# Performance work log

Hardware: AMD Instinct MI355X
Metric: run time of the kernel (lower is better)

The kernel has to match this reference:

```python
import jax, jax.numpy as jnp
import numpy as np

B, IDF, CDF, SIZE, H, L = 32, 64, 256, 32, 8, 256
SS = SIZE * SIZE  # size*size = 1024


def setup_inputs() -> dict:
    key = jax.random.key(0)
    k1, k2, k3 = jax.random.split(key, 3)
    return {
        "weightedContext": jax.random.normal(k1, (B, IDF, SS), dtype=jnp.float32),
        "context": jax.random.normal(k2, (B, CDF, L), dtype=jnp.float32),
        # per-head conv1x1 weights: [H, size*size, cdf]
        "W": jax.random.normal(k3, (H, SS, CDF), dtype=jnp.float32) * 0.02,
        "ih": SIZE,
        "iw": SIZE,
    }


def reference(weightedContext, context, W, ih, iw):
    batch, idf = weightedContext.shape[0], weightedContext.shape[1]
    # conv1x1 per head == per-head GEMM over channel dim: [B,H,SS,L]
    sourceC = jnp.einsum("hoc,bcl->bhol", W, context)
    # attention scores: [B,H,idf,L]
    attn = jnp.einsum("bio,bhol->bhil", weightedContext, sourceC)
    # softmax over sourceL (nn.Softmax() on 2D view -> dim=1 == L here)
    attn = jax.nn.softmax(attn, axis=-1)
    # weightedContext_T summed over heads: bmm(sourceC, attn^T) -> [B,idf,SS]
    ctx_out = jnp.einsum("bhol,bhil->bio", sourceC, attn)
    ctx_out = ctx_out.reshape(batch, idf, ih, iw)
    # attnOut: per-head attn transposed [B,L,idf], summed over heads
    attn_out = jnp.sum(attn, axis=1).transpose(0, 2, 1)
    return ctx_out, attn_out
```

## Files before the change

### kernel.cpp

```cpp
#include <hip/hip_runtime.h>
#include <hip/hip_bf16.h>

#define BB 32
#define IDF 64
#define CDF 256
#define SSZ 1024
#define NH 8
#define LL 256
#define KHC 2048

typedef __attribute__((ext_vector_type(8))) _Float16 half8v;
typedef __attribute__((ext_vector_type(4))) float f32x4;

#define GLDS16(g, l) __builtin_amdgcn_global_load_lds(                        \
    (const __attribute__((address_space(1))) void*)(g),                       \
    (__attribute__((address_space(3))) void*)(l), 16, 0, 0)

#define WAIT_ENTER3(NFULL, NHALF)                                             \
  { if (ks < NSTEP - 2)                                                       \
      asm volatile("s_waitcnt vmcnt(" #NFULL ")" ::: "memory");               \
    else if (ks == NSTEP - 2)                                                 \
      asm volatile("s_waitcnt vmcnt(" #NHALF ")" ::: "memory");               \
    else                                                                      \
      asm volatile("s_waitcnt vmcnt(0)" ::: "memory");                        \
    __builtin_amdgcn_s_barrier();                                             \
    __builtin_amdgcn_sched_barrier(0); }
#define BAR_EXIT()                                                            \
  { __builtin_amdgcn_sched_barrier(0);                                        \
    __builtin_amdgcn_s_barrier();                                             \
    __builtin_amdgcn_sched_barrier(0); }

__device__ inline unsigned short f2h(float x) {
  _Float16 h = (_Float16)x;
  return *reinterpret_cast<unsigned short*>(&h);
}
__device__ inline float h2f(unsigned short u) {
  _Float16 h = *reinterpret_cast<_Float16*>(&u);
  return (float)h;
}

__global__ __launch_bounds__(256) void k_split_all(const float* __restrict__ wc,
                                                   const float* __restrict__ W,
                                                   const float* __restrict__ ctx,
                                                   unsigned short* __restrict__ wc16,
                                                   unsigned short* __restrict__ W16,
                                                   unsigned short* __restrict__ ctx16) {
  int sel = blockIdx.x >> 11;
  int idx = ((blockIdx.x & 2047) * 256 + threadIdx.x) * 4;
  const float* src = (sel == 0) ? wc : (sel == 1) ? W : ctx;
  unsigned short* d = (sel == 0) ? wc16 : (sel == 1) ? W16 : ctx16;
  float4 v = *reinterpret_cast<const float4*>(&src[idx]);
  __align__(8) unsigned short h[4] = {f2h(v.x), f2h(v.y), f2h(v.z), f2h(v.w)};
  *reinterpret_cast<int2*>(&d[idx]) = *reinterpret_cast<int2*>(h);
}

__global__ __launch_bounds__(256) void k_split_T(const float* __restrict__ W,
                                                 const float* __restrict__ ctx,
                                                 unsigned short* __restrict__ wt,
                                                 unsigned short* __restrict__ ct) {
  __shared__ float Tt[64][65];
  int blk0 = blockIdx.x;
  int t = threadIdx.x;
  if (blk0 < 512) {
    int blk = blk0;
    int h = blk >> 6, ot = (blk >> 2) & 15, cq = blk & 3;
    int og = ot * 64, cg = cq * 64;
    int o_l = t >> 4, c4 = (t & 15) * 4;
#pragma unroll
    for (int p = 0; p < 4; ++p) {
      int o = o_l + 16 * p;
      float4 v = *reinterpret_cast<const float4*>(
          &W[((size_t)h * SSZ + og + o) * CDF + cg + c4]);
      Tt[c4 + 0][o] = v.x; Tt[c4 + 1][o] = v.y;
      Tt[c4 + 2][o] = v.z; Tt[c4 + 3][o] = v.w;
    }
    __syncthreads();
    int c_l = t >> 2;
#pragma unroll
    for (int p = 0; p < 4; ++p) {
      int o0 = ((t & 3) + 4 * p) * 4;
      __align__(8) unsigned short hv[4];
#pragma unroll
      for (int j = 0; j < 4; ++j) hv[j] = f2h(Tt[c_l][o0 + j]);
      size_t base = ((size_t)h * CDF + cg + c_l) * SSZ + og + o0;
      *reinterpret_cast<int2*>(&wt[base]) = *reinterpret_cast<int2*>(hv);
    }
  } else {
    int blk = blk0 - 512;
    int b = blk >> 4, cq = (blk >> 2) & 3, lt = blk & 3;
    int cg = cq * 64, lg = lt * 64;
    int c_l = t >> 4, l4 = (t & 15) * 4;
#pragma unroll
    for (int p = 0; p < 4; ++p) {
      int c = c_l + 16 * p;
      float4 v = *reinterpret_cast<const float4*>(
          &ctx[((size_t)b * CDF + cg + c) * LL + lg + l4]);
      Tt[l4 + 0][c] = v.x; Tt[l4 + 1][c] = v.y;
      Tt[l4 + 2][c] = v.z; Tt[l4 + 3][c] = v.w;
    }
    __syncthreads();
    int l_l = t >> 2;
#pragma unroll
    for (int p = 0; p < 4; ++p) {
      int c0 = ((t & 3) + 4 * p) * 4;
      __align__(8) unsigned short hv[4];
#pragma unroll
      for (int j = 0; j < 4; ++j) hv[j] = f2h(Tt[l_l][c0 + j]);
      size_t base = ((size_t)b * LL + lg + l_l) * CDF + cg + c0;
      *reinterpret_cast<int2*>(&ct[base]) = *reinterpret_cast<int2*>(hv);
    }
  }
}

__device__ __forceinline__ void k1_stage(short* dst,
                                         const short* gA, const short* gB,
                                         int wave, int lane, int k0) {
#pragma unroll
  for (int j = 0; j < 3; ++j) {
    int inst = wave * 3 + j;
    if (inst < 4) {
      int rb = inst * 16;
      int r  = rb + (lane >> 2);
      int gc = (lane & 3) ^ ((r >> 1) & 3);
      GLDS16(gA + (size_t)r * SSZ + k0 + gc * 8, dst + rb * 32);
    } else {
      int rb = (inst - 4) * 16;
      int r  = rb + (lane >> 2);
      int gc = (lane & 3) ^ ((r >> 1) & 3);
      GLDS16(gB + (size_t)r * SSZ + k0 + gc * 8, dst + 2048 + rb * 32);
    }
  }
}

__global__ __launch_bounds__(256) void k1_mfma(const unsigned short* __restrict__ wc16,
                                               const unsigned short* __restrict__ Wt16,
                                               unsigned short* __restrict__ M16) {
  __shared__ __align__(16) short S[3 * 6144];

  int blk = blockIdx.x;
  int bh = blk >> 1, nh = blk & 1;
  int b = bh >> 3, h = bh & 7;
  int t = threadIdx.x;
  int lane = t & 63, wave = t >> 6;
  int ln15 = lane & 15, kh = lane >> 4;

  const short* gA = (const short*)wc16 + (size_t)b * IDF * SSZ;
  const short* gB = (const short*)Wt16 + (size_t)(h * CDF + nh * 128) * SSZ;

  int offA[4], offB[2];
#pragma unroll
  for (int r = 0; r < 4; ++r) {
    int row = r * 16 + ln15;
    offA[r] = row * 32 + ((kh ^ ((row >> 1) & 3)) * 8);
  }
#pragma unroll
  for (int c = 0; c < 2; ++c) {
    int row = wave * 32 + c * 16 + ln15;
    offB[c] = 2048 + row * 32 + ((kh ^ ((row >> 1) & 3)) * 8);
  }

  f32x4 acc[4][2] = {};
  k1_stage(&S[0],        gA, gB, wave, lane, 0);
  k1_stage(&S[6144],     gA, gB, wave, lane, 32);
  k1_stage(&S[2 * 6144], gA, gB, wave, lane, 64);
  int cur = 0;

  const int NSTEP = 32;
#pragma unroll 1
  for (int ks = 0; ks < NSTEP; ++ks) {
    short* Sc = &S[cur * 6144];
    WAIT_ENTER3(6, 3)
    half8v fa[4], fb[2];
#pragma unroll
    for (int r = 0; r < 4; ++r)
      fa[r] = *reinterpret_cast<const half8v*>(&Sc[offA[r]]);
#pragma unroll
    for (int c = 0; c < 2; ++c)
      fb[c] = *reinterpret_cast<const half8v*>(&Sc[offB[c]]);
    __builtin_amdgcn_s_setprio(1);
#pragma unroll
    for (int r = 0; r < 4; ++r)
#pragma unroll
      for (int c = 0; c < 2; ++c)
        acc[r][c] = __builtin_amdgcn_mfma_f32_16x16x32_f16(fa[r], fb[c], acc[r][c], 0, 0, 0);
    __builtin_amdgcn_s_setprio(0);
    BAR_EXIT()
    if (ks + 3 < NSTEP)
      k1_stage(Sc, gA, gB, wave, lane, (ks + 3) * 32);
    cur = (cur == 2) ? 0 : cur + 1;
  }

  size_t obase = (size_t)bh * IDF * CDF + nh * 128;
  int rowq = (lane >> 4) * 4;
#pragma unroll
  for (int r = 0; r < 4; ++r)
#pragma unroll
    for (int c = 0; c < 2; ++c)
#pragma unroll
      for (int reg = 0; reg < 4; ++reg) {
        size_t idx = obase + (size_t)(r * 16 + rowq + reg) * CDF + wave * 32 + c * 16 + ln15;
        M16[idx] = f2h(acc[r][c][reg]);
      }
}

__device__ __forceinline__ void k2_stage(short* dst,
                                         const short* gM, const short* gT,
                                         int wave, int lane, int k0) {
#pragma unroll
  for (int j = 0; j < 3; ++j) {
    int inst = wave * 3 + j;
    const short* src; int tile_off, rb;
    if (inst < 4)       { src = gM; tile_off = 0;     rb = inst * 16; }
    else if (inst < 20) { src = gT; tile_off = 2048;  rb = (inst - 4) * 16; }
    else                { src = gM; tile_off = 10240; rb = (inst - 20) * 16; }
    int r  = rb + (lane >> 2);
    int gc = (lane & 3) ^ ((r >> 1) & 3);
    GLDS16(src + (size_t)r * CDF + k0 + gc * 8, dst + tile_off + rb * 32);
  }
}

__global__ __launch_bounds__(512) void k_attn(const unsigned short* __restrict__ M16,
                                              const unsigned short* __restrict__ cT16,
                                              unsigned short* __restrict__ P16) {
  __shared__ __align__(16) short S[3 * 12288];

  int bh = blockIdx.x;
  int b = bh >> 3;
  int t = threadIdx.x;
  int lane = t & 63, wave = t >> 6;
  int ln15 = lane & 15, kh = lane >> 4;

  const short* gM = (const short*)M16 + (size_t)bh * IDF * CDF;
  const short* gT = (const short*)cT16 + (size_t)b * LL * CDF;

  int offA[4], offB[2];
#pragma unroll
  for (int r = 0; r < 4; ++r) {
    int row = r * 16 + ln15;
    offA[r] = row * 32 + ((kh ^ ((row >> 1) & 3)) * 8);
  }
#pragma unroll
  for (int c = 0; c < 2; ++c) {
    int row = wave * 32 + c * 16 + ln15;
    offB[c] = 2048 + row * 32 + ((kh ^ ((row >> 1) & 3)) * 8);
  }

  f32x4 acc[4][2] = {};
  k2_stage(&S[0],         gM, gT, wave, lane, 0);
  k2_stage(&S[12288],     gM, gT, wave, lane, 32);
  k2_stage(&S[2 * 12288], gM, gT, wave, lane, 64);
  int cur = 0;

  const int NSTEP = 8;
#pragma unroll 1
  for (int ks = 0; ks < NSTEP; ++ks) {
    short* Sc = &S[cur * 12288];
    WAIT_ENTER3(6, 3)
    half8v fa[4], fb[2];
#pragma unroll
    for (int r = 0; r < 4; ++r)
      fa[r] = *reinterpret_cast<const half8v*>(&Sc[offA[r]]);
#pragma unroll
    for (int c = 0; c < 2; ++c)
      fb[c] = *reinterpret_cast<const half8v*>(&Sc[offB[c]]);
    __builtin_amdgcn_s_setprio(1);
#pragma unroll
    for (int r = 0; r < 4; ++r)
#pragma unroll
      for (int c = 0; c < 2; ++c)
        acc[r][c] = __builtin_amdgcn_mfma_f32_16x16x32_f16(fa[r], fb[c], acc[r][c], 0, 0, 0);
    __builtin_amdgcn_s_setprio(0);
    BAR_EXIT()
    if (ks + 3 < NSTEP)
      k2_stage(Sc, gM, gT, wave, lane, (ks + 3) * 32);
    cur = (cur == 2) ? 0 : cur + 1;
  }

  float* pm = reinterpret_cast<float*>(&S[0]);
  int rowq = (lane >> 4) * 4;
  float gmax[4][4], ginv[4][4];
#pragma unroll
  for (int r = 0; r < 4; ++r)
#pragma unroll
    for (int reg = 0; reg < 4; ++reg) {
      float m = fmaxf(acc[r][0][reg], acc[r][1][reg]);
#pragma unroll
      for (int msk = 8; msk >= 1; msk >>= 1) m = fmaxf(m, __shfl_xor(m, msk, 64));
      if (ln15 == 0) pm[(r * 16 + rowq + reg) * 8 + wave] = m;
    }
  __syncthreads();
#pragma unroll
  for (int r = 0; r < 4; ++r)
#pragma unroll
    for (int reg = 0; reg < 4; ++reg) {
      int row = r * 16 + rowq + reg;
      float4 p0 = *reinterpret_cast<const float4*>(&pm[row * 8]);
      float4 p1 = *reinterpret_cast<const float4*>(&pm[row * 8 + 4]);
      gmax[r][reg] = fmaxf(fmaxf(fmaxf(p0.x, p0.y), fmaxf(p0.z, p0.w)),
                           fmaxf(fmaxf(p1.x, p1.y), fmaxf(p1.z, p1.w)));
    }
  __syncthreads();
#pragma unroll
  for (int r = 0; r < 4; ++r)
#pragma unroll
    for (int reg = 0; reg < 4; ++reg) {
      acc[r][0][reg] = __expf(acc[r][0][reg] - gmax[r][reg]);
      acc[r][1][reg] = __expf(acc[r][1][reg] - gmax[r][reg]);
      float s = acc[r][0][reg] + acc[r][1][reg];
#pragma unroll
      for (int msk = 8; msk >= 1; msk >>= 1) s += __shfl_xor(s, msk, 64);
      if (ln15 == 0) pm[(r * 16 + rowq + reg) * 8 + wave] = s;
    }
  __syncthreads();
#pragma unroll
  for (int r = 0; r < 4; ++r)
#pragma unroll
    for (int reg = 0; reg < 4; ++reg) {
      int row = r * 16 + rowq + reg;
      float4 p0 = *reinterpret_cast<const float4*>(&pm[row * 8]);
      float4 p1 = *reinterpret_cast<const float4*>(&pm[row * 8 + 4]);
      ginv[r][reg] = 1.f / (p0.x + p0.y + p0.z + p0.w + p1.x + p1.y + p1.z + p1.w);
    }
  size_t obase = (size_t)bh * IDF * LL;
#pragma unroll
  for (int r = 0; r < 4; ++r)
#pragma unroll
    for (int c = 0; c < 2; ++c)
#pragma unroll
      for (int reg = 0; reg < 4; ++reg) {
        float p = acc[r][c][reg] * ginv[r][reg];
        size_t idx = obase + (size_t)(r * 16 + rowq + reg) * LL + wave * 32 + c * 16 + ln15;
        P16[idx] = f2h(p);
      }
}

__device__ __forceinline__ void k3_stage(short* dst,
                                         const short* gP, const short* gC,
                                         int wave, int lane, int k0) {
#pragma unroll
  for (int j = 0; j < 3; ++j) {
    int inst = wave * 3 + j;
    const short* src; int tile_off, rb;
    if (inst < 4) { src = gP; tile_off = 0;    rb = inst * 16; }
    else          { src = gC; tile_off = 2048; rb = (inst - 4) * 16; }
    int r  = rb + (lane >> 2);
    int gc = (lane & 3) ^ ((r >> 1) & 3);
    GLDS16(src + (size_t)r * LL + k0 + gc * 8, dst + tile_off + rb * 32);
  }
}

__global__ __launch_bounds__(256) void k_N2(const unsigned short* __restrict__ P16,
                                            const unsigned short* __restrict__ ctx16,
                                            unsigned short* __restrict__ N216) {
  __shared__ __align__(16) short S[3 * 6144];

  int blk = blockIdx.x;
  int bh = blk >> 1, ch = blk & 1;
  int b = bh >> 3, h = bh & 7;
  int cgbase = ch * 128;
  int t = threadIdx.x;
  int lane = t & 63, wave = t >> 6;
  int ln15 = lane & 15, kh = lane >> 4;

  const short* gP = (const short*)P16 + (size_t)bh * IDF * LL;
  const short* gC = (const short*)ctx16 + (size_t)(b * CDF + cgbase) * LL;

  int offA[4], offB[2];
#pragma unroll
  for (int r = 0; r < 4; ++r) {
    int row = r * 16 + ln15;
    offA[r] = row * 32 + ((kh ^ ((row >> 1) & 3)) * 8);
  }
#pragma unroll
  for (int c = 0; c < 2; ++c) {
    int row = wave * 32 + c * 16 + ln15;
    offB[c] = 2048 + row * 32 + ((kh ^ ((row >> 1) & 3)) * 8);
  }

  f32x4 acc[4][2] = {};
  k3_stage(&S[0],        gP, gC, wave, lane, 0);
  k3_stage(&S[6144],     gP, gC, wave, lane, 32);
  k3_stage(&S[2 * 6144], gP, gC, wave, lane, 64);
  int cur = 0;

  const int NSTEP = 8;
#pragma unroll 1
  for (int ks = 0; ks < NSTEP; ++ks) {
    short* Sc = &S[cur * 6144];
    WAIT_ENTER3(6, 3)
    half8v fa[4], fb[2];
#pragma unroll
    for (int r = 0; r < 4; ++r)
      fa[r] = *reinterpret_cast<const half8v*>(&Sc[offA[r]]);
#pragma unroll
    for (int c = 0; c < 2; ++c)
      fb[c] = *reinterpret_cast<const half8v*>(&Sc[offB[c]]);
    __builtin_amdgcn_s_setprio(1);
#pragma unroll
    for (int r = 0; r < 4; ++r)
#pragma unroll
      for (int c = 0; c < 2; ++c)
        acc[r][c] = __builtin_amdgcn_mfma_f32_16x16x32_f16(fa[r], fb[c], acc[r][c], 0, 0, 0);
    __builtin_amdgcn_s_setprio(0);
    BAR_EXIT()
    if (ks + 3 < NSTEP)
      k3_stage(Sc, gP, gC, wave, lane, (ks + 3) * 32);
    cur = (cur == 2) ? 0 : cur + 1;
  }

  size_t base = (size_t)b * IDF * KHC + h * CDF + cgbase;
  int rowq = (lane >> 4) * 4;
#pragma unroll
  for (int r = 0; r < 4; ++r)
#pragma unroll
    for (int c = 0; c < 2; ++c)
#pragma unroll
      for (int reg = 0; reg < 4; ++reg) {
        size_t idx = base + (size_t)(r * 16 + rowq + reg) * KHC + wave * 32 + c * 16 + ln15;
        N216[idx] = f2h(acc[r][c][reg]);
      }
}

__device__ __forceinline__ void k4_stage(short* dst,
                                         const short* gA, const short* gB,
                                         int wave, int lane, int kk0, int obase) {
  int h4 = kk0 >> 8, cb = kk0 & 255;
#pragma unroll
  for (int j = 0; j < 3; ++j) {
    int inst = wave * 3 + j;
    if (inst < 4) {
      int rb = inst * 16;
      int r  = rb + (lane >> 2);
      int gc = (lane & 3) ^ ((r >> 1) & 3);
      GLDS16(gA + (size_t)r * KHC + kk0 + gc * 8, dst + rb * 32);
    } else {
      int rb = (inst - 4) * 16;
      int r  = rb + (lane >> 2);
      int gc = (lane & 3) ^ ((r >> 1) & 3);
      GLDS16(gB + (size_t)(h4 * SSZ + obase + r) * CDF + cb + gc * 8,
             dst + 2048 + rb * 32);
    }
  }
}

__global__ __launch_bounds__(256) void k4_mfma(const unsigned short* __restrict__ N216,
                                               const unsigned short* __restrict__ W16,
                                               float* __restrict__ out0,
                                               float* __restrict__ out1) {
  __shared__ __align__(16) short S[3 * 6144];

  int blk = blockIdx.x;
  int g = blk >> 8;
  int r8 = blk & 255;
  int b = r8 >> 3, ot = r8 & 7;
  int obase = ot * 128;
  int t = threadIdx.x;
  int lane = t & 63, wave = t >> 6;
  int ln15 = lane & 15, kh = lane >> 4;

  const short* gA = (const short*)N216 + (size_t)b * IDF * KHC;
  const short* gB = (const short*)W16;

  int offA[4], offB[2];
#pragma unroll
  for (int r = 0; r < 4; ++r) {
    int row = r * 16 + ln15;
    offA[r] = row * 32 + ((kh ^ ((row >> 1) & 3)) * 8);
  }
#pragma unroll
  for (int c = 0; c < 2; ++c) {
    int row = wave * 32 + c * 16 + ln15;
    offB[c] = 2048 + row * 32 + ((kh ^ ((row >> 1) & 3)) * 8);
  }

  int kbase = g * (KHC / 2);
  f32x4 acc[4][2] = {};

  k4_stage(&S[0],        gA, gB, wave, lane, kbase, obase);
  k4_stage(&S[6144],     gA, gB, wave, lane, kbase + 32, obase);
  k4_stage(&S[2 * 6144], gA, gB, wave, lane, kbase + 64, obase);
  int cur = 0;

  const int NSTEP = 32;
#pragma unroll 1
  for (int ks = 0; ks < NSTEP; ++ks) {
    short* Sc = &S[cur * 6144];
    WAIT_ENTER3(6, 3)
    half8v fa[4], fb[2];
#pragma unroll
    for (int r = 0; r < 4; ++r)
      fa[r] = *reinterpret_cast<const half8v*>(&Sc[offA[r]]);
#pragma unroll
    for (int c = 0; c < 2; ++c)
      fb[c] = *reinterpret_cast<const half8v*>(&Sc[offB[c]]);
    __builtin_amdgcn_s_setprio(1);
#pragma unroll
    for (int r = 0; r < 4; ++r)
#pragma unroll
      for (int c = 0; c < 2; ++c)
        acc[r][c] = __builtin_amdgcn_mfma_f32_16x16x32_f16(fa[r], fb[c], acc[r][c], 0, 0, 0);
    __builtin_amdgcn_s_setprio(0);
    BAR_EXIT()
    if (ks + 3 < NSTEP)
      k4_stage(Sc, gA, gB, wave, lane, kbase + (ks + 3) * 32, obase);
    cur = (cur == 2) ? 0 : cur + 1;
  }

  float* dst = (g == 0) ? out0 : out1;
  int rowq = (lane >> 4) * 4;
#pragma unroll
  for (int r = 0; r < 4; ++r)
#pragma unroll
    for (int c = 0; c < 2; ++c)
#pragma unroll
      for (int reg = 0; reg < 4; ++reg)
        dst[((size_t)b * IDF + r * 16 + rowq + reg) * SSZ +
            obase + wave * 32 + c * 16 + ln15] = acc[r][c][reg];
}

__global__ __launch_bounds__(256) void k_epi(const unsigned short* __restrict__ P16,
                                             float* __restrict__ outa,
                                             float* __restrict__ out,
                                             const float* __restrict__ Pbuf) {
  int blk0 = blockIdx.x;
  int tid = threadIdx.x;
  if (blk0 >= 128) {
    int idx = (blk0 - 128) * 256 + tid;
    float4 a = reinterpret_cast<float4*>(out)[idx];
    float4 p = reinterpret_cast<const float4*>(Pbuf)[idx];
    a.x += p.x; a.y += p.y; a.z += p.z; a.w += p.w;
    reinterpret_cast<float4*>(out)[idx] = a;
    return;
  }
  __shared__ float T[64][65];
  int b = blk0 >> 2, lt = blk0 & 3;
  int l0 = lt * 64;
  float4 acc[4];
#pragma unroll
  for (int p = 0; p < 4; ++p) acc[p] = make_float4(0.f, 0.f, 0.f, 0.f);
  for (int h = 0; h < NH; ++h) {
    size_t src = (size_t)(b * NH + h) * IDF * LL;
#pragma unroll
    for (int p = 0; p < 4; ++p) {
      int f = tid + p * 256;
      int i = f >> 4, lc = (f & 15) * 4;
      ushort4 u = *reinterpret_cast<const ushort4*>(&P16[src + i * LL + l0 + lc]);
      acc[p].x += h2f(u.x); acc[p].y += h2f(u.y);
      acc[p].z += h2f(u.z); acc[p].w += h2f(u.w);
    }
  }
#pragma unroll
  for (int p = 0; p < 4; ++p) {
    int f = tid + p * 256;
    int i = f >> 4, lc = (f & 15) * 4;
    T[i][lc + 0] = acc[p].x; T[i][lc + 1] = acc[p].y;
    T[i][lc + 2] = acc[p].z; T[i][lc + 3] = acc[p].w;
  }
  __syncthreads();
#pragma unroll
  for (int p = 0; p < 4; ++p) {
    int f = tid + p * 256;
    int lr = f >> 4, ic = (f & 15) * 4;
    float4 v = {T[ic + 0][lr], T[ic + 1][lr], T[ic + 2][lr], T[ic + 3][lr]};
    *reinterpret_cast<float4*>(&outa[((size_t)b * LL + l0 + lr) * IDF + ic]) = v;
  }
}

extern "C" void kernel_launch(void* const* d_in, const int* in_sizes, int n_in,
                              void* d_out, int out_size, void* d_ws, size_t ws_size,
                              hipStream_t stream) {
  const float* wc  = (const float*)d_in[0];
  const float* ctx = (const float*)d_in[1];
  const float* W   = (const float*)d_in[2];
  float* out = (float*)d_out;

  const size_t NE = 2097152;
  const size_t NM = 4194304;
  unsigned short* p = (unsigned short*)d_ws;
  unsigned short *wc16 = p;   p += NE;
  unsigned short *Wt16 = p;   p += NE;
  unsigned short *W16  = p;   p += NE;
  unsigned short *ctx16 = p;  p += NE;
  unsigned short *cT16 = p;   p += NE;
  unsigned short *M16  = p;   p += NM;
  unsigned short *P16  = p;   p += NM;
  unsigned short *N216 = p;   p += NM;
  float* Pbuf = (float*)p;

  k_split_all <<<6144, 256, 0, stream>>>(wc, W, ctx, wc16, W16, ctx16);
  k_split_T   <<<1024, 256, 0, stream>>>(W, ctx, Wt16, cT16);
  k1_mfma     <<<BB * NH * 2, 256, 0, stream>>>(wc16, Wt16, M16);
  k_attn      <<<BB * NH, 512, 0, stream>>>(M16, cT16, P16);
  k_N2        <<<BB * NH * 2, 256, 0, stream>>>(P16, ctx16, N216);
  k4_mfma     <<<512, 256, 0, stream>>>(N216, W16, out, Pbuf);
  k_epi       <<<2176, 256, 0, stream>>>(P16, out + (size_t)BB * IDF * SSZ, out, Pbuf);
}
```

Before: 84.16 us.

## Fuse three attention GEMM stages into one kernel with M kept in LDS

Merges the two fp16 conversion/transposition kernels into one prep launch. Fuses the projection GEMM, the score GEMM with softmax, and the N2 GEMM into a single 512-thread kernel per (batch, head). The intermediate M and the probabilities are held in swizzled LDS instead of going through global memory, which removes the M16 buffer and several launches. In exchange the grid drops from 512 blocks to 256 and each block needs much more LDS, so occupancy falls and the stages inside a block run one after another.

```diff
diff --git a/kernel.cpp b/kernel.cpp
--- a/kernel.cpp
+++ b/kernel.cpp
@@ -29,6 +29,10 @@
   { __builtin_amdgcn_sched_barrier(0);                                        \
     __builtin_amdgcn_s_barrier();                                             \
     __builtin_amdgcn_sched_barrier(0); }
+#define LDS_BAR()                                                             \
+  { asm volatile("s_waitcnt lgkmcnt(0)" ::: "memory");                        \
+    __builtin_amdgcn_s_barrier();                                             \
+    __builtin_amdgcn_sched_barrier(0); }
 
 __device__ inline unsigned short f2h(float x) {
   _Float16 h = (_Float16)x;
@@ -39,30 +43,27 @@
   return (float)h;
 }
 
-__global__ __launch_bounds__(256) void k_split_all(const float* __restrict__ wc,
-                                                   const float* __restrict__ W,
-                                                   const float* __restrict__ ctx,
-                                                   unsigned short* __restrict__ wc16,
-                                                   unsigned short* __restrict__ W16,
-                                                   unsigned short* __restrict__ ctx16) {
-  int sel = blockIdx.x >> 11;
-  int idx = ((blockIdx.x & 2047) * 256 + threadIdx.x) * 4;
-  const float* src = (sel == 0) ? wc : (sel == 1) ? W : ctx;
-  unsigned short* d = (sel == 0) ? wc16 : (sel == 1) ? W16 : ctx16;
-  float4 v = *reinterpret_cast<const float4*>(&src[idx]);
-  __align__(8) unsigned short h[4] = {f2h(v.x), f2h(v.y), f2h(v.z), f2h(v.w)};
-  *reinterpret_cast<int2*>(&d[idx]) = *reinterpret_cast<int2*>(h);
-}
-
-__global__ __launch_bounds__(256) void k_split_T(const float* __restrict__ W,
-                                                 const float* __restrict__ ctx,
-                                                 unsigned short* __restrict__ wt,
-                                                 unsigned short* __restrict__ ct) {
+__global__ __launch_bounds__(256) void k_prep(const float* __restrict__ wc,
+                                              const float* __restrict__ W,
+                                              const float* __restrict__ ctx,
+                                              unsigned short* __restrict__ wc16,
+                                              unsigned short* __restrict__ W16,
+                                              unsigned short* __restrict__ ctx16,
+                                              unsigned short* __restrict__ Wt16,
+                                              unsigned short* __restrict__ cT16) {
   __shared__ float Tt[64][65];
   int blk0 = blockIdx.x;
   int t = threadIdx.x;
-  if (blk0 < 512) {
-    int blk = blk0;
+  if (blk0 < 6144) {
+    int sel = blk0 >> 11;
+    int idx = ((blk0 & 2047) * 256 + t) * 4;
+    const float* src = (sel == 0) ? wc : (sel == 1) ? W : ctx;
+    unsigned short* d = (sel == 0) ? wc16 : (sel == 1) ? W16 : ctx16;
+    float4 v = *reinterpret_cast<const float4*>(&src[idx]);
+    __align__(8) unsigned short h[4] = {f2h(v.x), f2h(v.y), f2h(v.z), f2h(v.w)};
+    *reinterpret_cast<int2*>(&d[idx]) = *reinterpret_cast<int2*>(h);
+  } else if (blk0 < 6656) {
+    int blk = blk0 - 6144;
     int h = blk >> 6, ot = (blk >> 2) & 15, cq = blk & 3;
     int og = ot * 64, cg = cq * 64;
     int o_l = t >> 4, c4 = (t & 15) * 4;
@@ -83,10 +84,10 @@
 #pragma unroll
       for (int j = 0; j < 4; ++j) hv[j] = f2h(Tt[c_l][o0 + j]);
       size_t base = ((size_t)h * CDF + cg + c_l) * SSZ + og + o0;
-      *reinterpret_cast<int2*>(&wt[base]) = *reinterpret_cast<int2*>(hv);
+      *reinterpret_cast<int2*>(&Wt16[base]) = *reinterpret_cast<int2*>(hv);
     }
   } else {
-    int blk = blk0 - 512;
+    int blk = blk0 - 6656;
     int b = blk >> 4, cq = (blk >> 2) & 3, lt = blk & 3;
     int cg = cq * 64, lg = lt * 64;
     int c_l = t >> 4, l4 = (t & 15) * 4;
@@ -107,51 +108,65 @@
 #pragma unroll
       for (int j = 0; j < 4; ++j) hv[j] = f2h(Tt[l_l][c0 + j]);
       size_t base = ((size_t)b * LL + lg + l_l) * CDF + cg + c0;
-      *reinterpret_cast<int2*>(&ct[base]) = *reinterpret_cast<int2*>(hv);
-    }
-  }
-}
-
-__device__ __forceinline__ void k1_stage(short* dst,
-                                         const short* gA, const short* gB,
-                                         int wave, int lane, int k0) {
+      *reinterpret_cast<int2*>(&cT16[base]) = *reinterpret_cast<int2*>(hv);
+    }
+  }
+}
+
+__device__ __forceinline__ void st_p1(short* dst, const short* gA, const short* gB,
+                                      int wave, int lane, int k0) {
 #pragma unroll
   for (int j = 0; j < 3; ++j) {
     int inst = wave * 3 + j;
-    if (inst < 4) {
-      int rb = inst * 16;
-      int r  = rb + (lane >> 2);
-      int gc = (lane & 3) ^ ((r >> 1) & 3);
-      GLDS16(gA + (size_t)r * SSZ + k0 + gc * 8, dst + rb * 32);
-    } else {
-      int rb = (inst - 4) * 16;
-      int r  = rb + (lane >> 2);
-      int gc = (lane & 3) ^ ((r >> 1) & 3);
-      GLDS16(gB + (size_t)r * SSZ + k0 + gc * 8, dst + 2048 + rb * 32);
-    }
-  }
-}
-
-__global__ __launch_bounds__(256) void k1_mfma(const unsigned short* __restrict__ wc16,
-                                               const unsigned short* __restrict__ Wt16,
-                                               unsigned short* __restrict__ M16) {
-  __shared__ __align__(16) short S[3 * 6144];
-
-  int blk = blockIdx.x;
-  int bh = blk >> 1, nh = blk & 1;
+    const short* src; int toff, rb;
+    if (inst < 4)       { src = gA; toff = 0;     rb = inst * 16; }
+    else if (inst < 20) { src = gB; toff = 2048;  rb = (inst - 4) * 16; }
+    else                { src = gA; toff = 10240; rb = (inst - 20) * 16; }
+    int r  = rb + (lane >> 2);
+    int gc = (lane & 3) ^ ((r >> 1) & 3);
+    GLDS16(src + (size_t)r * SSZ + k0 + gc * 8, dst + toff + rb * 32);
+  }
+}
+__device__ __forceinline__ void st_pB(short* dst, const short* gB, int ld,
+                                      int wave, int lane, int k0) {
+#pragma unroll
+  for (int j = 0; j < 2; ++j) {
+    int inst = wave * 2 + j;
+    int rb = inst * 16;
+    int r  = rb + (lane >> 2);
+    int gc = (lane & 3) ^ ((r >> 1) & 3);
+    GLDS16(gB + (size_t)r * ld + k0 + gc * 8, dst + 2048 + rb * 32);
+  }
+}
+
+__global__ __launch_bounds__(512) void k123(const unsigned short* __restrict__ wc16,
+                                            const unsigned short* __restrict__ Wt16,
+                                            const unsigned short* __restrict__ cT16,
+                                            const unsigned short* __restrict__ ctx16,
+                                            unsigned short* __restrict__ P16,
+                                            unsigned short* __restrict__ N216) {
+  __shared__ __align__(16) short S[3 * 12288 + 16384];
+  short* M_lds = &S[3 * 12288];
+
+  int bh = blockIdx.x;
   int b = bh >> 3, h = bh & 7;
   int t = threadIdx.x;
   int lane = t & 63, wave = t >> 6;
   int ln15 = lane & 15, kh = lane >> 4;
+  int rowq = (lane >> 4) * 4;
 
   const short* gA = (const short*)wc16 + (size_t)b * IDF * SSZ;
-  const short* gB = (const short*)Wt16 + (size_t)(h * CDF + nh * 128) * SSZ;
-
-  int offA[4], offB[2];
+  const short* gB = (const short*)Wt16 + (size_t)h * CDF * SSZ;
+  const short* gT = (const short*)cT16 + (size_t)b * LL * CDF;
+  const short* gC = (const short*)ctx16 + (size_t)b * CDF * LL;
+
+  int offA[4], offB[2], rowM[4], rmask[4];
 #pragma unroll
   for (int r = 0; r < 4; ++r) {
     int row = r * 16 + ln15;
     offA[r] = row * 32 + ((kh ^ ((row >> 1) & 3)) * 8);
+    rowM[r] = row * 256;
+    rmask[r] = row & 7;
   }
 #pragma unroll
   for (int c = 0; c < 2; ++c) {
@@ -160,124 +175,92 @@
   }
 
   f32x4 acc[4][2] = {};
-  k1_stage(&S[0],        gA, gB, wave, lane, 0);
-  k1_stage(&S[6144],     gA, gB, wave, lane, 32);
-  k1_stage(&S[2 * 6144], gA, gB, wave, lane, 64);
+
+  st_p1(&S[0],         gA, gB, wave, lane, 0);
+  st_p1(&S[12288],     gA, gB, wave, lane, 32);
+  st_p1(&S[2 * 12288], gA, gB, wave, lane, 64);
   int cur = 0;
-
-  const int NSTEP = 32;
+  {
+    const int NSTEP = 32;
 #pragma unroll 1
-  for (int ks = 0; ks < NSTEP; ++ks) {
-    short* Sc = &S[cur * 6144];
-    WAIT_ENTER3(6, 3)
-    half8v fa[4], fb[2];
-#pragma unroll
-    for (int r = 0; r < 4; ++r)
-      fa[r] = *reinterpret_cast<const half8v*>(&Sc[offA[r]]);
+    for (int ks = 0; ks < NSTEP; ++ks) {
+      short* Sc = &S[cur * 12288];
+      WAIT_ENTER3(6, 3)
+      half8v fa[4], fb[2];
+#pragma unroll
+      for (int r = 0; r < 4; ++r)
+        fa[r] = *reinterpret_cast<const half8v*>(&Sc[offA[r]]);
+#pragma unroll
+      for (int c = 0; c < 2; ++c)
+        fb[c] = *reinterpret_cast<const half8v*>(&Sc[offB[c]]);
+      __builtin_amdgcn_s_setprio(1);
+#pragma unroll
+      for (int r = 0; r < 4; ++r)
+#pragma unroll
+        for (int c = 0; c < 2; ++c)
+          acc[r][c] = __builtin_amdgcn_mfma_f32_16x16x32_f16(fa[r], fb[c], acc[r][c], 0, 0, 0);
+      __builtin_amdgcn_s_setprio(0);
+      BAR_EXIT()
+      if (ks + 3 < NSTEP)
+        st_p1(Sc, gA, gB, wave, lane, (ks + 3) * 32);
+      cur = (cur == 2) ? 0 : cur + 1;
+    }
+  }
+#pragma unroll
+  for (int r = 0; r < 4; ++r)
 #pragma unroll
     for (int c = 0; c < 2; ++c)
-      fb[c] = *reinterpret_cast<const half8v*>(&Sc[offB[c]]);
-    __builtin_amdgcn_s_setprio(1);
-#pragma unroll
-    for (int r = 0; r < 4; ++r)
+#pragma unroll
+      for (int reg = 0; reg < 4; ++reg) {
+        int row = r * 16 + rowq + reg;
+        int col = wave * 32 + c * 16 + ln15;
+        M_lds[row * 256 + ((((col >> 3) ^ (row & 7)) << 3) + (col & 7))] =
+            (short)f2h(acc[r][c][reg]);
+      }
+  LDS_BAR()
+
+#pragma unroll
+  for (int r = 0; r < 4; ++r)
+#pragma unroll
+    for (int c = 0; c < 2; ++c) acc[r][c] = (f32x4){0.f, 0.f, 0.f, 0.f};
+  st_pB(&S[0],         gT, CDF, wave, lane, 0);
+  st_pB(&S[12288],     gT, CDF, wave, lane, 32);
+  st_pB(&S[2 * 12288], gT, CDF, wave, lane, 64);
+  cur = 0;
+  {
+    const int NSTEP = 8;
+#pragma unroll 1
+    for (int ks = 0; ks < NSTEP; ++ks) {
+      short* Sc = &S[cur * 12288];
+      WAIT_ENTER3(4, 2)
+      half8v fa[4], fb[2];
+#pragma unroll
+      for (int r = 0; r < 4; ++r) {
+        int ck = ((ks * 4 + kh) ^ rmask[r]) << 3;
+        fa[r] = *reinterpret_cast<const half8v*>(&M_lds[rowM[r] + ck]);
+      }
 #pragma unroll
       for (int c = 0; c < 2; ++c)
-        acc[r][c] = __builtin_amdgcn_mfma_f32_16x16x32_f16(fa[r], fb[c], acc[r][c], 0, 0, 0);
-    __builtin_amdgcn_s_setprio(0);
-    BAR_EXIT()
-    if (ks + 3 < NSTEP)
-      k1_stage(Sc, gA, gB, wave, lane, (ks + 3) * 32);
-    cur = (cur == 2) ? 0 : cur + 1;
-  }
-
-  size_t obase = (size_t)bh * IDF * CDF + nh * 128;
-  int rowq = (lane >> 4) * 4;
-#pragma unroll
-  for (int r = 0; r < 4; ++r)
-#pragma unroll
-    for (int c = 0; c < 2; ++c)
-#pragma unroll
-      for (int reg = 0; reg < 4; ++reg) {
-        size_t idx = obase + (size_t)(r * 16 + rowq + reg) * CDF + wave * 32 + c * 16 + ln15;
-        M16[idx] = f2h(acc[r][c][reg]);
-      }
-}
-
-__device__ __forceinline__ void k2_stage(short* dst,
-                                         const short* gM, const short* gT,
-                                         int wave, int lane, int k0) {
-#pragma unroll
-  for (int j = 0; j < 3; ++j) {
-    int inst = wave * 3 + j;
-    const short* src; int tile_off, rb;
-    if (inst < 4)       { src = gM; tile_off = 0;     rb = inst * 16; }
-    else if (inst < 20) { src = gT; tile_off = 2048;  rb = (inst - 4) * 16; }
-    else                { src = gM; tile_off = 10240; rb = (inst - 20) * 16; }
-    int r  = rb + (lane >> 2);
-    int gc = (lane & 3) ^ ((r >> 1) & 3);
-    GLDS16(src + (size_t)r * CDF + k0 + gc * 8, dst + tile_off + rb * 32);
-  }
-}
-
-__global__ __launch_bounds__(512) void k_attn(const unsigned short* __restrict__ M16,
-                                              const unsigned short* __restrict__ cT16,
-                                              unsigned short* __restrict__ P16) {
-  __shared__ __align__(16) short S[3 * 12288];
-
-  int bh = blockIdx.x;
-  int b = bh >> 3;
-  int t = threadIdx.x;
-  int lane = t & 63, wave = t >> 6;
-  int ln15 = lane & 15, kh = lane >> 4;
-
-  const short* gM = (const short*)M16 + (size_t)bh * IDF * CDF;
-  const short* gT = (const short*)cT16 + (size_t)b * LL * CDF;
-
-  int offA[4], offB[2];
-#pragma unroll
-  for (int r = 0; r < 4; ++r) {
-    int row = r * 16 + ln15;
-    offA[r] = row * 32 + ((kh ^ ((row >> 1) & 3)) * 8);
-  }
-#pragma unroll
-  for (int c = 0; c < 2; ++c) {
-    int row = wave * 32 + c * 16 + ln15;
-    offB[c] = 2048 + row * 32 + ((kh ^ ((row >> 1) & 3)) * 8);
-  }
-
-  f32x4 acc[4][2] = {};
-  k2_stage(&S[0],         gM, gT, wave, lane, 0);
-  k2_stage(&S[12288],     gM, gT, wave, lane, 32);
-  k2_stage(&S[2 * 12288], gM, gT, wave, lane, 64);
-  int cur = 0;
-
-  const int NSTEP = 8;
-#pragma unroll 1
-  for (int ks = 0; ks < NSTEP; ++ks) {
-    short* Sc = &S[cur * 12288];
-    WAIT_ENTER3(6, 3)
-    half8v fa[4], fb[2];
-#pragma unroll
-    for (int r = 0; r < 4; ++r)
-      fa[r] = *reinterpret_cast<const half8v*>(&Sc[offA[r]]);
-#pragma unroll
-    for (int c = 0; c < 2; ++c)
-      fb[c] = *reinterpret_cast<const half8v*>(&Sc[offB[c]]);
-    __builtin_amdgcn_s_setprio(1);
-#pragma unroll
-    for (int r = 0; r < 4; ++r)
-#pragma unroll
-      for (int c = 0; c < 2; ++c)
-        acc[r][c] = __builtin_amdgcn_mfma_f32_16x16x32_f16(fa[r], fb[c], acc[r][c], 0, 0, 0);
-    __builtin_amdgcn_s_setprio(0);
-    BAR_EXIT()
-    if (ks + 3 < NSTEP)
-      k2_stage(Sc, gM, gT, wave, lane, (ks + 3) * 32);
-    cur = (cur == 2) ? 0 : cur + 1;
-  }
-
-  float* pm = reinterpret_cast<float*>(&S[0]);
-  int rowq = (lane >> 4) * 4;
+        fb[c] = *reinterpret_cast<const half8v*>(&Sc[offB[c]]);
+      __builtin_amdgcn_s_setprio(1);
+#pragma unroll
+      for (int r = 0; r < 4; ++r)
+#pragma unroll
+        for (int c = 0; c < 2; ++c)
+          acc[r][c] = __builtin_amdgcn_mfma_f32_16x16x32_f16(fa[r], fb[c], acc[r][c], 0, 0, 0);
+      __builtin_amdgcn_s_setprio(0);
+      BAR_EXIT()
+      if (ks + 3 < NSTEP)
+        st_pB(Sc, gT, CDF, wave, lane, (ks + 3) * 32);
+      cur = (cur == 2) ? 0 : cur + 1;
+    }
+  }
+
+  st_pB(&S[0],         gC, LL, wave, lane, 0);
+  st_pB(&S[12288],     gC, LL, wave, lane, 32);
+  st_pB(&S[2 * 12288], gC, LL, wave, lane, 64);
+
+  float* pm = reinterpret_cast<float*>(M_lds);
   float gmax[4][4], ginv[4][4];
 #pragma unroll
   for (int r = 0; r < 4; ++r)
@@ -288,7 +271,7 @@
       for (int msk = 8; msk >= 1; msk >>= 1) m = fmaxf(m, __shfl_xor(m, msk, 64));
       if (ln15 == 0) pm[(r * 16 + rowq + reg) * 8 + wave] = m;
     }
-  __syncthreads();
+  LDS_BAR()
 #pragma unroll
   for (int r = 0; r < 4; ++r)
 #pragma unroll
@@ -299,7 +282,7 @@
       gmax[r][reg] = fmaxf(fmaxf(fmaxf(p0.x, p0.y), fmaxf(p0.z, p0.w)),
                            fmaxf(fmaxf(p1.x, p1.y), fmaxf(p1.z, p1.w)));
     }
-  __syncthreads();
+  LDS_BAR()
 #pragma unroll
   for (int r = 0; r < 4; ++r)
 #pragma unroll
@@ -311,7 +294,7 @@
       for (int msk = 8; msk >= 1; msk >>= 1) s += __shfl_xor(s, msk, 64);
       if (ln15 == 0) pm[(r * 16 + rowq + reg) * 8 + wave] = s;
     }
-  __syncthreads();
+  LDS_BAR()
 #pragma unroll
   for (int r = 0; r < 4; ++r)
 #pragma unroll
@@ -321,7 +304,9 @@
       float4 p1 = *reinterpret_cast<const float4*>(&pm[row * 8 + 4]);
       ginv[r][reg] = 1.f / (p0.x + p0.y + p0.z + p0.w + p1.x + p1.y + p1.z + p1.w);
     }
-  size_t obase = (size_t)bh * IDF * LL;
+  LDS_BAR()
+
+  size_t pbase = (size_t)bh * IDF * LL;
 #pragma unroll
   for (int r = 0; r < 4; ++r)
 #pragma unroll
@@ -329,94 +314,56 @@
 #pragma unroll
       for (int reg = 0; reg < 4; ++reg) {
         float p = acc[r][c][reg] * ginv[r][reg];
-        size_t idx = obase + (size_t)(r * 16 + rowq + reg) * LL + wave * 32 + c * 16 + ln15;
-        P16[idx] = f2h(p);
+        int row = r * 16 + rowq + reg;
+        int col = wave * 32 + c * 16 + ln15;
+        unsigned short ph = f2h(p);
+        P16[pbase + (size_t)row * LL + col] = ph;
+        M_lds[row * 256 + ((((col >> 3) ^ (row & 7)) << 3) + (col & 7))] = (short)ph;
       }
-}
-
-__device__ __forceinline__ void k3_stage(short* dst,
-                                         const short* gP, const short* gC,
-                                         int wave, int lane, int k0) {
-#pragma unroll
-  for (int j = 0; j < 3; ++j) {
-    int inst = wave * 3 + j;
-    const short* src; int tile_off, rb;
-    if (inst < 4) { src = gP; tile_off = 0;    rb = inst * 16; }
-    else          { src = gC; tile_off = 2048; rb = (inst - 4) * 16; }
-    int r  = rb + (lane >> 2);
-    int gc = (lane & 3) ^ ((r >> 1) & 3);
-    GLDS16(src + (size_t)r * LL + k0 + gc * 8, dst + tile_off + rb * 32);
-  }
-}
-
-__global__ __launch_bounds__(256) void k_N2(const unsigned short* __restrict__ P16,
-                                            const unsigned short* __restrict__ ctx16,
-                                            unsigned short* __restrict__ N216) {
-  __shared__ __align__(16) short S[3 * 6144];
-
-  int blk = blockIdx.x;
-  int bh = blk >> 1, ch = blk & 1;
-  int b = bh >> 3, h = bh & 7;
-  int cgbase = ch * 128;
-  int t = threadIdx.x;
-  int lane = t & 63, wave = t >> 6;
-  int ln15 = lane & 15, kh = lane >> 4;
-
-  const short* gP = (const short*)P16 + (size_t)bh * IDF * LL;
-  const short* gC = (const short*)ctx16 + (size_t)(b * CDF + cgbase) * LL;
-
-  int offA[4], offB[2];
-#pragma unroll
-  for (int r = 0; r < 4; ++r) {
-    int row = r * 16 + ln15;
-    offA[r] = row * 32 + ((kh ^ ((row >> 1) & 3)) * 8);
-  }
-#pragma unroll
-  for (int c = 0; c < 2; ++c) {
-    int row = wave * 32 + c * 16 + ln15;
-    offB[c] = 2048 + row * 32 + ((kh ^ ((row >> 1) & 3)) * 8);
-  }
-
-  f32x4 acc[4][2] = {};
-  k3_stage(&S[0],        gP, gC, wave, lane, 0);
-  k3_stage(&S[6144],     gP, gC, wave, lane, 32);
-  k3_stage(&S[2 * 6144], gP, gC, wave, lane, 64);
-  int cur = 0;
-
-  const int NSTEP = 8;
+  LDS_BAR()
+
+#pragma unroll
+  for (int r = 0; r < 4; ++r)
+#pragma unroll
+    for (int c = 0; c < 2; ++c) acc[r][c] = (f32x4){0.f, 0.f, 0.f, 0.f};
+  cur = 0;
+  {
+    const int NSTEP = 8;
 #pragma unroll 1
-  for (int ks = 0; ks < NSTEP; ++ks) {
-    short* Sc = &S[cur * 6144];
-    WAIT_ENTER3(6, 3)
-    half8v fa[4], fb[2];
-#pragma unroll
-    for (int r = 0; r < 4; ++r)
-      fa[r] = *reinterpret_cast<const half8v*>(&Sc[offA[r]]);
+    for (int ks = 0; ks < NSTEP; ++ks) {
+      short* Sc = &S[cur * 12288];
+      WAIT_ENTER3(4, 2)
+      half8v fa[4], fb[2];
+#pragma unroll
+      for (int r = 0; r < 4; ++r) {
+        int ck = ((ks * 4 + kh) ^ rmask[r]) << 3;
+        fa[r] = *reinterpret_cast<const half8v*>(&M_lds[rowM[r] + ck]);
+      }
+#pragma unroll
+      for (int c = 0; c < 2; ++c)
+        fb[c] = *reinterpret_cast<const half8v*>(&Sc[offB[c]]);
+      __builtin_amdgcn_s_setprio(1);
+#pragma unroll
+      for (int r = 0; r < 4; ++r)
+#pragma unroll
+        for (int c = 0; c < 2; ++c)
+          acc[r][c] = __builtin_amdgcn_mfma_f32_16x16x32_f16(fa[r], fb[c], acc[r][c], 0, 0, 0);
+      __builtin_amdgcn_s_setprio(0);
+      BAR_EXIT()
+      if (ks + 3 < NSTEP)
+        st_pB(Sc, gC, LL, wave, lane, (ks + 3) * 32);
+      cur = (cur == 2) ? 0 : cur + 1;
+    }
+  }
+
+  size_t nbase = (size_t)b * IDF * KHC + h * CDF;
+#pragma unroll
+  for (int r = 0; r < 4; ++r)
 #pragma unroll
     for (int c = 0; c < 2; ++c)
-      fb[c] = *reinterpret_cast<const half8v*>(&Sc[offB[c]]);
-    __builtin_amdgcn_s_setprio(1);
-#pragma unroll
-    for (int r = 0; r < 4; ++r)
-#pragma unroll
-      for (int c = 0; c < 2; ++c)
-        acc[r][c] = __builtin_amdgcn_mfma_f32_16x16x32_f16(fa[r], fb[c], acc[r][c], 0, 0, 0);
-    __builtin_amdgcn_s_setprio(0);
-    BAR_EXIT()
-    if (ks + 3 < NSTEP)
-      k3_stage(Sc, gP, gC, wave, lane, (ks + 3) * 32);
-    cur = (cur == 2) ? 0 : cur + 1;
-  }
-
-  size_t base = (size_t)b * IDF * KHC + h * CDF + cgbase;
-  int rowq = (lane >> 4) * 4;
-#pragma unroll
-  for (int r = 0; r < 4; ++r)
-#pragma unroll
-    for (int c = 0; c < 2; ++c)
 #pragma unroll
       for (int reg = 0; reg < 4; ++reg) {
-        size_t idx = base + (size_t)(r * 16 + rowq + reg) * KHC + wave * 32 + c * 16 + ln15;
+        size_t idx = nbase + (size_t)(r * 16 + rowq + reg) * KHC + wave * 32 + c * 16 + ln15;
         N216[idx] = f2h(acc[r][c][reg]);
       }
 }
@@ -582,16 +529,12 @@
   unsigned short *W16  = p;   p += NE;
   unsigned short *ctx16 = p;  p += NE;
   unsigned short *cT16 = p;   p += NE;
-  unsigned short *M16  = p;   p += NM;
   unsigned short *P16  = p;   p += NM;
   unsigned short *N216 = p;   p += NM;
   float* Pbuf = (float*)p;
 
-  k_split_all <<<6144, 256, 0, stream>>>(wc, W, ctx, wc16, W16, ctx16);
-  k_split_T   <<<1024, 256, 0, stream>>>(W, ctx, Wt16, cT16);
-  k1_mfma     <<<BB * NH * 2, 256, 0, stream>>>(wc16, Wt16, M16);
-  k_attn      <<<BB * NH, 512, 0, stream>>>(M16, cT16, P16);
-  k_N2        <<<BB * NH * 2, 256, 0, stream>>>(P16, ctx16, N216);
-  k4_mfma     <<<512, 256, 0, stream>>>(N216, W16, out, Pbuf);
-  k_epi       <<<2176, 256, 0, stream>>>(P16, out + (size_t)BB * IDF * SSZ, out, Pbuf);
-}
+  k_prep  <<<7168, 256, 0, stream>>>(wc, W, ctx, wc16, W16, ctx16, Wt16, cT16);
+  k123    <<<BB * NH, 512, 0, stream>>>(wc16, Wt16, cT16, ctx16, P16, N216);
+  k4_mfma <<<512, 256, 0, stream>>>(N216, W16, out, Pbuf);
+  k_epi   <<<2176, 256, 0, stream>>>(P16, out + (size_t)BB * IDF * SSZ, out, Pbuf);
+}
```

After: 79.78 us. 1.05x faster.
